# Kernel tuning notes

Hardware: AMD Instinct MI355X
Metric: run time of the kernel (lower is better)

Reference implementation:

```python
import jax, jax.numpy as jnp
from jax import lax
import numpy as np

PS = 3      # patch_size
PROP = 3    # propagate_size
DN = ('NCHW', 'OIHW', 'NCHW')


def _conv1x1(x, W, b):
    # x: [b, c, h, w]; W: [o, c]; 1x1 conv == channel matmul
    return jnp.einsum('oc,bchw->bohw', W, x) + b[None, :, None, None]


def _mpga(q_in, k_in, mask, Wq, bq, Wk, bk, Wv, bv):
    # q_in/k_in: [b, c, w, h], mask: [b, 1, w, h] (already at feature resolution)
    b, c, w, h = q_in.shape
    kp = _conv1x1(k_in, Wk, bk).reshape(b, c, w * h)          # [b, c, wh]
    qp = _conv1x1(q_in, Wq, bq).reshape(b, c, w * h)          # [b, c, wh]
    scores = jnp.einsum('bci,bcj->bij', qp, kp)               # [b, wh_q, wh_k]
    mrow = mask.reshape(b, w * h)[:, :, None]                 # mask over query rows
    A = jax.nn.softmax(scores * mrow, axis=-1)                # softmax over keys
    vp = _conv1x1(k_in, Wv, bv).reshape(b, c, w * h)
    out = jnp.einsum('bcj,bij->bci', vp, A).reshape(b, c, w, h)
    return q_in * mask + (1.0 - mask) * out


def _gap(x, m, Wq, bq, Wk, bk, Wv, bv, gamma):
    # GlobalAttentionPatch on patch stacks: x, m: [N, c, ps, ps]
    N, c, ph, pw = x.shape
    q = jnp.einsum('oc,ncij->noij', Wq, x) + bq[None, :, None, None]
    k = jnp.einsum('oc,ncij->noij', Wk, x) + bk[None, :, None, None]
    v = jnp.einsum('oc,ncij->noij', Wv, x) + bv[None, :, None, None]
    qf, kf, vf, mf = (t.reshape(N, c, ph * pw) for t in (q, k, v, m))
    cc = jnp.einsum('ncp,ndp->ncd', qf, kf)                   # [N, c, c]
    cc = jnp.einsum('ncd,ndp->ncp', cc, mf)                   # [N, c, ps*ps]
    energy = jax.nn.softmax(cc, axis=-1)
    att = (energy * vf).reshape(N, c, ph, pw)
    return x * m + gamma * (1.0 - m) * att


def _patches(x, ps):
    # torch: pad(ps//2) -> unfold(2, ps, 1).unfold(3, ps, 1) -> [b, N=w*h, c, ps, ps]
    b, c, w, h = x.shape
    p = ps // 2
    xp = jnp.pad(x, ((0, 0), (0, 0), (p, p), (p, p)))
    sl = [xp[:, :, di:di + w, dj:dj + h] for di in range(ps) for dj in range(ps)]
    pat = jnp.stack(sl, axis=-1).reshape(b, c, w, h, ps, ps)
    return pat.reshape(b, c, w * h, ps, ps).transpose(0, 2, 1, 3, 4)


def _gla_forward(foreground, mask, pf, pp, gamma):
    background = foreground * (1.0 - mask)
    fg = _mpga(foreground, background, mask, *pf)
    ck_all = _patches(background, PS)                          # [b, N, c, 3, 3]
    mk_all = _patches(jnp.broadcast_to(mask, foreground.shape), PS)
    pad = [(PS // 2, PS // 2)] * 2

    def per_sample(fm, ck, mk):
        # fm: [c, w, h]; ck, mk: [N, c, 3, 3]
        ck = ck + 1e-7
        ck = _gap(ck, mk, *pp, gamma)
        ck = ck / jnp.sqrt(jnp.sum(ck ** 2, axis=(1, 2, 3), keepdims=True))
        cr = lax.conv_general_dilated(fm[None], ck, (1, 1), pad,
                                      dimension_numbers=DN)    # [1, N, w, h]
        N = ck.shape[0]
        prop_k = jnp.ones((N, 1, PROP, PROP), fm.dtype)        # depthwise ones
        cr = lax.conv_general_dilated(cr, prop_k, (1, 1), [(1, 1), (1, 1)],
                                      dimension_numbers=DN, feature_group_count=N)
        mm = (jnp.mean(mk, axis=(1, 2, 3)) == 0.0).astype(fm.dtype)[None, :, None, None]
        att = jax.nn.softmax(cr * mm, axis=1) * mm             # softmax over N patches
        # conv_transpose2d(att, ck, stride=1, padding=1) == conv with flipped, swapped kernel
        Wt = jnp.flip(ck, (2, 3)).transpose(1, 0, 2, 3)        # [c, N, 3, 3]
        rec = lax.conv_general_dilated(att, Wt, (1, 1), pad, dimension_numbers=DN)
        return rec[0]

    return jax.vmap(per_sample)(fg, ck_all, mk_all)


def setup_inputs() -> dict:
    key = jax.random.key(0)
    ks = jax.random.split(key, 8)
    bz, nc, w, h = 2, 64, 64, 64
    s = 0.02
    foreground = jax.random.normal(ks[0], (bz, nc, w, h), jnp.float32)
    mask = jnp.zeros((bz, 1, w, h), jnp.float32).at[:, :, 16:48, 16:48].set(1.0)

    def lin(k):
        kw, kb = jax.random.split(k)
        return (jax.random.normal(kw, (nc, nc), jnp.float32) * s,
                jax.random.normal(kb, (nc,), jnp.float32) * s)

    Wq_f, bq_f = lin(ks[1]); Wk_f, bk_f = lin(ks[2]); Wv_f, bv_f = lin(ks[3])
    Wq_p, bq_p = lin(ks[4]); Wk_p, bk_p = lin(ks[5]); Wv_p, bv_p = lin(ks[6])
    return dict(foreground=foreground, mask=mask, same_number_of_args=0,
                Wq_f=Wq_f, bq_f=bq_f, Wk_f=Wk_f, bk_f=bk_f, Wv_f=Wv_f, bv_f=bv_f,
                Wq_p=Wq_p, bq_p=bq_p, Wk_p=Wk_p, bk_p=bk_p, Wv_p=Wv_p, bv_p=bv_p,
                gamma=jnp.ones((1,), jnp.float32))


def reference(foreground, mask, same_number_of_args,
              Wq_f, bq_f, Wk_f, bk_f, Wv_f, bv_f,
              Wq_p, bq_p, Wk_p, bk_p, Wv_p, bv_p, gamma):
    del same_number_of_args  # unused by the torch module as well
    pf = (Wq_f, bq_f, Wk_f, bk_f, Wv_f, bv_f)
    pp = (Wq_p, bq_p, Wk_p, bk_p, Wv_p, bv_p)
    return _gla_forward(foreground, mask, pf, pp, gamma)
```

## Files before the change

### kernel.cpp

```cpp
#include <hip/hip_runtime.h>


#define BSZ 2
#define C 64
#define WD 64
#define WH 4096
#define PW 66
#define PP 4356
#define KC 576
#define NP 4096

typedef unsigned short u16;
typedef unsigned int u32;
typedef short bf16x8 __attribute__((ext_vector_type(8)));
typedef float f32x4 __attribute__((ext_vector_type(4)));

__device__ inline u16 bf16_rne(float x) {
  unsigned u = __float_as_uint(x);
  return (u16)((u + 0x7FFFu + ((u >> 16) & 1u)) >> 16);
}
__device__ inline float bf16_tof(u16 h) { return __uint_as_float(((unsigned)h) << 16); }
__device__ inline void split2(float x, u16& h, u16& l) {
  h = bf16_rne(x);
  l = bf16_rne(x - bf16_tof(h));
}
__device__ inline u32 pack2(float x) {
  u16 h, l;
  split2(x, h, l);
  return ((u32)h << 16) | (u32)l;
}


__global__ void k_mu(const float* __restrict__ fg, const float* __restrict__ mask,
                     float* __restrict__ mu) {
  int bc = blockIdx.x;
  int b = bc >> 6;
  const float* f = fg + (size_t)bc * WH;
  const float* mk = mask + (size_t)b * WH;
  float sum = 0.f;
  for (int i = threadIdx.x; i < WH; i += 256) sum += f[i] * (1.f - mk[i]);
  __shared__ float red[256];
  red[threadIdx.x] = sum;
  __syncthreads();
  for (int s = 128; s > 0; s >>= 1) {
    if (threadIdx.x < s) red[threadIdx.x] += red[threadIdx.x + s];
    __syncthreads();
  }
  if (threadIdx.x == 0) mu[bc] = red[0] / (float)WH;
}

__global__ void k_vmean(const float* __restrict__ Wv_f, const float* __restrict__ bv_f,
                        const float* __restrict__ mu, float* __restrict__ vmean) {
  int t = threadIdx.x;
  int b = t >> 6, c = t & 63;
  float acc = bv_f[c];
  for (int cc = 0; cc < C; ++cc) acc += Wv_f[c * C + cc] * mu[b * C + cc];
  vmean[t] = acc;
}

__global__ void k_fm(const float* __restrict__ fg, const float* __restrict__ mask,
                     const float* __restrict__ vmean, float* __restrict__ fm) {
  int idx = blockIdx.x * 256 + threadIdx.x;
  if (idx >= BSZ * C * WH) return;
  int b = idx >> 18;
  int c = (idx >> 12) & 63;
  int pos = idx & (WH - 1);
  float m = mask[b * WH + pos];
  fm[idx] = fg[idx] * m + (1.f - m) * vmean[b * C + c];
}

__global__ void k_bgpT(const float* __restrict__ fg, const float* __restrict__ mask,
                       float* __restrict__ bgp) {
  int b = blockIdx.y, xp = blockIdx.x;
  float* out = bgp + ((size_t)b * PP + (size_t)xp * PW) * C;
  int t = threadIdx.x;
  __shared__ float tile[64][65];
  int xi = xp - 1;
  if (xi >= 0 && xi < WD) {
    const float* fgb = fg + (size_t)b * C * WH + (size_t)xi * WD;
    const float* mkb = mask + (size_t)b * WH + (size_t)xi * WD;
    for (int i = t; i < 64 * 64; i += 256) {
      int c = i >> 6, y = i & 63;
      tile[c][y] = fgb[(size_t)c * WH + y] * (1.f - mkb[y]);
    }
  }
  __syncthreads();
  for (int i = t; i < PW * C; i += 256) {
    int yp = i >> 6, c = i & 63;
    float v = 1e-7f;
    int yj = yp - 1;
    if (xi >= 0 && xi < WD && yj >= 0 && yj < WD) v += tile[c][yj];
    out[(size_t)yp * C + c] = v;
  }
}

__global__ void k_vgT(const float* __restrict__ bgp, const float* __restrict__ Wv_p,
                      const float* __restrict__ bv_p, float* __restrict__ Vg) {
  __shared__ float Wt[64][65];
  __shared__ float bgl[4][64];
  int t = threadIdx.x;
  for (int i = t; i < 4096; i += 256) Wt[i & 63][i >> 6] = Wv_p[i];
  int pos0 = blockIdx.x * 4;
  {
    int p2 = t >> 6, c = t & 63;
    int gp = pos0 + p2;
    bgl[p2][c] = (gp < BSZ * PP) ? bgp[(size_t)gp * C + c] : 0.f;
  }
  __syncthreads();
  int pi = t >> 6, o = t & 63;
  int gpos = pos0 + pi;
  if (gpos < BSZ * PP) {
    float acc = bv_p[o];
    for (int c = 0; c < 64; ++c) acc += Wt[c][o] * bgl[pi][c];
    Vg[(size_t)gpos * C + o] = acc;
  }
}

__global__ void k_mmf(const float* __restrict__ mask, float* __restrict__ mmf) {
  int idx = blockIdx.x * 256 + threadIdx.x;
  if (idx >= BSZ * NP) return;
  int b = idx >> 12, n = idx & 4095;
  int x = n >> 6, y = n & 63;
  float z = 0.f;
  for (int di = -1; di <= 1; ++di)
    for (int dj = -1; dj <= 1; ++dj) {
      int xi = x + di, yj = y + dj;
      if (xi >= 0 && xi < WD && yj >= 0 && yj < WD) z += mask[b * WH + xi * WD + yj];
    }
  mmf[idx] = (z == 0.f) ? 1.f : 0.f;
}

__global__ void k_scan(const float* __restrict__ mmf, int* __restrict__ lividx,
                       int* __restrict__ nliv) {
  int b = blockIdx.x, t = threadIdx.x;
  const float* mm = mmf + (size_t)b * NP;
  int* li = lividx + (size_t)b * NP;
  __shared__ int cnt[256];
  int loc[16];
  int c = 0;
#pragma unroll
  for (int i = 0; i < 16; ++i) {
    int lv = (mm[t * 16 + i] != 0.f) ? 1 : 0;
    loc[i] = lv;
    c += lv;
  }
  cnt[t] = c;
  __syncthreads();
  for (int s = 1; s < 256; s <<= 1) {
    int v = (t >= s) ? cnt[t - s] : 0;
    __syncthreads();
    cnt[t] += v;
    __syncthreads();
  }
  int base = cnt[t] - c;
#pragma unroll
  for (int i = 0; i < 16; ++i)
    if (loc[i]) li[base++] = t * 16 + i;
  int nl = cnt[255];
  if (t == 0) nliv[b] = nl;
  for (int i = nl + t; i < NP; i += 256) li[i] = 0;
}

__global__ void k_ck(const float* __restrict__ Vg, const int* __restrict__ lividx,
                     const int* __restrict__ nliv, const float* __restrict__ gamma,
                     u16* __restrict__ AkcH, u16* __restrict__ AkcL) {
  int b = blockIdx.y, nc = blockIdx.x;
  if (nc >= nliv[b]) return;
  int n = lividx[(size_t)b * NP + nc];
  int x = n >> 6, y = n & 63;
  int c = threadIdx.x;
  const float* vg = Vg + (size_t)b * PP * C;
  float g9 = gamma[0] * (1.f / 9.f);
  float o[9];
  float ss = 0.f;
#pragma unroll
  for (int p = 0; p < 9; ++p) {
    int di = p / 3, dj = p % 3;
    float v = g9 * vg[(size_t)((x + di) * PW + (y + dj)) * C + c];
    o[p] = v;
    ss += v * v;
  }
#pragma unroll
  for (int off = 32; off > 0; off >>= 1) ss += __shfl_down(ss, off, 64);
  ss = __shfl(ss, 0, 64);
  float rn = 1.f / sqrtf(ss);
  u16* ph = AkcH + ((size_t)b * NP + nc) * KC + c * 9;
  u16* pl = AkcL + ((size_t)b * NP + nc) * KC + c * 9;
#pragma unroll
  for (int p = 0; p < 9; ++p) {
    u16 h, l;
    split2(o[p] * rn, h, l);
    ph[p] = h;
    pl[p] = l;
  }
}

__global__ void k_trA(const u16* __restrict__ Sh, const u16* __restrict__ Sl,
                      u16* __restrict__ Dh, u16* __restrict__ Dl) {
  __shared__ __align__(16) u16 tile[64][72];
  int x0 = blockIdx.x * 64, k0 = blockIdx.y * 64;
  int t = threadIdx.x;
  for (int pass = 0; pass < 2; ++pass) {
    const u16* S = pass ? Sl : Sh;
    u16* D = pass ? Dl : Dh;
    for (int ch = t; ch < 512; ch += 256) {
      int r = ch >> 3, c0 = (ch & 7) * 8;
      *reinterpret_cast<uint4*>(&tile[r][c0]) =
          *reinterpret_cast<const uint4*>(S + (size_t)(x0 + r) * KC + k0 + c0);
    }
    __syncthreads();
    for (int ch = t; ch < 512; ch += 256) {
      int kr = ch >> 3, c0 = (ch & 7) * 8;
      union { u16 u[8]; uint4 v; } pk;
#pragma unroll
      for (int j = 0; j < 8; ++j) pk.u[j] = tile[c0 + j][kr];
      *reinterpret_cast<uint4*>(D + (size_t)(k0 + kr) * NP + x0 + c0) = pk.v;
    }
    __syncthreads();
  }
}

__global__ void k_im2colT(const float* __restrict__ fm, u16* __restrict__ base) {
  int ch = blockIdx.x * 256 + threadIdx.x;
  if (ch >= BSZ * WH * 72) return;
  int b = ch / (WH * 72);
  int rem = ch - b * WH * 72;
  int xy = rem / 72, kp = rem - xy * 72;
  int x = xy >> 6, y = xy & 63;
  union { u16 u[8]; uint4 v; } H, L;
#pragma unroll
  for (int j = 0; j < 8; ++j) {
    int k = kp * 8 + j;
    int c = k / 9, p = k - c * 9;
    int xi = x + p / 3 - 1, yj = y + p % 3 - 1;
    float v = 0.f;
    if (xi >= 0 && xi < WD && yj >= 0 && yj < WD)
      v = fm[((size_t)(b * C + c)) * WH + (xi << 6) + yj];
    split2(v, H.u[j], L.u[j]);
  }
  u16* bh = base + (size_t)b * 2 * WH * KC;
  u16* bl = bh + (size_t)WH * KC;
  *reinterpret_cast<uint4*>(bh + (size_t)xy * KC + kp * 8) = H.v;
  *reinterpret_cast<uint4*>(bl + (size_t)xy * KC + kp * 8) = L.v;
}


__global__ __launch_bounds__(256, 4) void k_gemmA(
    const u16* __restrict__ Ah, const u16* __restrict__ Al,
    const u16* __restrict__ Bh, const u16* __restrict__ Bl,
    const int* __restrict__ nliv, float* __restrict__ Cp) {
  int nl = *nliv;
  int m0 = blockIdx.y * 128;
  if (m0 >= nl) return;
  int n0 = blockIdx.x * 64;
  __shared__ __align__(16) u16 As[2][128][40];
  __shared__ __align__(16) u16 Bs[2][64][40];
  int t = threadIdx.x;
  f32x4 zero = {0.f, 0.f, 0.f, 0.f};
  f32x4 acc[2][4];
#pragma unroll
  for (int r = 0; r < 2; ++r)
#pragma unroll
    for (int c = 0; c < 4; ++c) acc[r][c] = zero;
  int l = t & 63, w = t >> 6;
  int lr = l & 15, lk = (l >> 4) * 8;
  for (int k0 = 0; k0 < KC; k0 += 32) {
    __syncthreads();
    for (int ch = t; ch < 1536; ch += 256) {
      const u16* src;
      u16* dst;
      if (ch < 1024) {
        int hl = ch >> 9, r = (ch >> 2) & 127, p = ch & 3;
        src = (hl ? Al : Ah) + (size_t)(m0 + r) * KC + k0 + p * 8;
        dst = &As[hl][r][p * 8];
      } else {
        int c2 = ch - 1024;
        int hl = c2 >> 8, r = (c2 >> 2) & 63, p = c2 & 3;
        src = (hl ? Bl : Bh) + (size_t)(n0 + r) * KC + k0 + p * 8;
        dst = &Bs[hl][r][p * 8];
      }
      *reinterpret_cast<uint4*>(dst) = *reinterpret_cast<const uint4*>(src);
    }
    __syncthreads();
    bf16x8 ah[2], al2[2], bh[4], bl2[4];
#pragma unroll
    for (int r = 0; r < 2; ++r) {
      ah[r] = *reinterpret_cast<const bf16x8*>(&As[0][32 * w + 16 * r + lr][lk]);
      al2[r] = *reinterpret_cast<const bf16x8*>(&As[1][32 * w + 16 * r + lr][lk]);
    }
#pragma unroll
    for (int c = 0; c < 4; ++c) {
      bh[c] = *reinterpret_cast<const bf16x8*>(&Bs[0][16 * c + lr][lk]);
      bl2[c] = *reinterpret_cast<const bf16x8*>(&Bs[1][16 * c + lr][lk]);
    }
#pragma unroll
    for (int r = 0; r < 2; ++r)
#pragma unroll
      for (int c = 0; c < 4; ++c) {
        acc[r][c] = __builtin_amdgcn_mfma_f32_16x16x32_bf16(ah[r], bh[c], acc[r][c], 0, 0, 0);
        acc[r][c] = __builtin_amdgcn_mfma_f32_16x16x32_bf16(ah[r], bl2[c], acc[r][c], 0, 0, 0);
        acc[r][c] = __builtin_amdgcn_mfma_f32_16x16x32_bf16(al2[r], bh[c], acc[r][c], 0, 0, 0);
      }
  }
#pragma unroll
  for (int r = 0; r < 2; ++r)
#pragma unroll
    for (int c = 0; c < 4; ++c)
#pragma unroll
      for (int q = 0; q < 4; ++q) {
        int row = m0 + 32 * w + 16 * r + ((l >> 4) << 2) + q;
        Cp[(size_t)row * WH + n0 + 16 * c + lr] = acc[r][c][q];
      }
}

__global__ __launch_bounds__(256, 4) void k_gemmB(
    const u16* __restrict__ Ah, const u16* __restrict__ Al,
    const u32* __restrict__ att32, const int* __restrict__ nliv,
    float* __restrict__ Cp) {
  int nl = *nliv;
  int Kend = (nl + 31) & ~31;
  int m0 = blockIdx.y * 64;
  int n0 = blockIdx.x * 64;
  __shared__ __align__(16) u16 As[2][64][40];
  __shared__ __align__(16) u16 Bs[2][64][40];
  __shared__ __align__(16) u32 Bfu[32][70];
  int t = threadIdx.x;
  f32x4 zero = {0.f, 0.f, 0.f, 0.f};
  f32x4 acc[4];
#pragma unroll
  for (int c = 0; c < 4; ++c) acc[c] = zero;
  int l = t & 63, w = t >> 6;
  int lr = l & 15, lk = (l >> 4) * 8;
  for (int k0 = 0; k0 < Kend; k0 += 32) {
    __syncthreads();
    for (int ch = t; ch < 512; ch += 256) {
      int hl = ch >> 8, r = (ch >> 2) & 63, p = ch & 3;
      const u16* src = (hl ? Al : Ah) + (size_t)(m0 + r) * NP + k0 + p * 8;
      *reinterpret_cast<uint4*>(&As[hl][r][p * 8]) = *reinterpret_cast<const uint4*>(src);
    }
    {
      int r = t >> 3, c0 = (t & 7) * 8;
      int krow = k0 + r;
      uint4 w0 = {0u, 0u, 0u, 0u}, w1 = {0u, 0u, 0u, 0u};
      if (krow < nl) {
        const u32* bp = att32 + (size_t)krow * WH + n0 + c0;
        w0 = *reinterpret_cast<const uint4*>(bp);
        w1 = *reinterpret_cast<const uint4*>(bp + 4);
      }
      Bfu[r][c0 + 0] = w0.x; Bfu[r][c0 + 1] = w0.y;
      Bfu[r][c0 + 2] = w0.z; Bfu[r][c0 + 3] = w0.w;
      Bfu[r][c0 + 4] = w1.x; Bfu[r][c0 + 5] = w1.y;
      Bfu[r][c0 + 6] = w1.z; Bfu[r][c0 + 7] = w1.w;
    }
    __syncthreads();
    {
      int n = t >> 2, kq = (t & 3) * 8;
      union { u16 u[8]; uint4 v; } H, L;
#pragma unroll
      for (int j = 0; j < 8; ++j) {
        u32 v = Bfu[kq + j][n];
        H.u[j] = (u16)(v >> 16);
        L.u[j] = (u16)(v & 0xFFFFu);
      }
      *reinterpret_cast<uint4*>(&Bs[0][n][kq]) = H.v;
      *reinterpret_cast<uint4*>(&Bs[1][n][kq]) = L.v;
    }
    __syncthreads();
    bf16x8 ah, al2, bh[4], bl2[4];
    ah = *reinterpret_cast<const bf16x8*>(&As[0][16 * w + lr][lk]);
    al2 = *reinterpret_cast<const bf16x8*>(&As[1][16 * w + lr][lk]);
#pragma unroll
    for (int c = 0; c < 4; ++c) {
      bh[c] = *reinterpret_cast<const bf16x8*>(&Bs[0][16 * c + lr][lk]);
      bl2[c] = *reinterpret_cast<const bf16x8*>(&Bs[1][16 * c + lr][lk]);
    }
#pragma unroll
    for (int c = 0; c < 4; ++c) {
      acc[c] = __builtin_amdgcn_mfma_f32_16x16x32_bf16(ah, bh[c], acc[c], 0, 0, 0);
      acc[c] = __builtin_amdgcn_mfma_f32_16x16x32_bf16(ah, bl2[c], acc[c], 0, 0, 0);
      acc[c] = __builtin_amdgcn_mfma_f32_16x16x32_bf16(al2, bh[c], acc[c], 0, 0, 0);
    }
  }
#pragma unroll
  for (int c = 0; c < 4; ++c)
#pragma unroll
    for (int q = 0; q < 4; ++q) {
      int row = m0 + 16 * w + ((l >> 4) << 2) + q;
      Cp[(size_t)row * WH + n0 + 16 * c + lr] = acc[c][q];
    }
}


__global__ __launch_bounds__(256) void k_box(const int* __restrict__ nliv,
                                             float* __restrict__ cr) {
  if ((int)blockIdx.x >= *nliv) return;
  __shared__ __align__(16) float sIn[WH];
  __shared__ __align__(16) float sT[WH];
  float* row = cr + (size_t)blockIdx.x * WH;
  const float4* r4 = reinterpret_cast<const float4*>(row);
  float4* s4 = reinterpret_cast<float4*>(sIn);
  for (int i = threadIdx.x; i < WH / 4; i += 256) s4[i] = r4[i];
  __syncthreads();
  for (int i = threadIdx.x; i < WH; i += 256) {
    int y = i & 63;
    float v = sIn[i];
    if (y > 0) v += sIn[i - 1];
    if (y < 63) v += sIn[i + 1];
    sT[i] = v;
  }
  __syncthreads();
  for (int i = threadIdx.x; i < WH; i += 256) {
    int x = i >> 6;
    float v = sT[i];
    if (x > 0) v += sT[i - 64];
    if (x < 63) v += sT[i + 64];
    row[i] = v;
  }
}

__global__ __launch_bounds__(256) void k_colstat(const float* __restrict__ cr,
                                                 const int* __restrict__ nliv,
                                                 float* __restrict__ pmax,
                                                 float* __restrict__ psum) {
  int xy = blockIdx.x * 256 + threadIdx.x;
  int nl = *nliv;
  int ns = (nl + 15) >> 4;
  int r0 = blockIdx.y * ns;
  int r1 = min(r0 + ns, nl);
  float mx = -3.4e38f, s = 0.f;
  for (int r = r0; r < r1; ++r) {
    float v = cr[(size_t)r * WH + xy];
    if (v <= mx) {
      s += __expf(v - mx);
    } else {
      s = s * __expf(mx - v) + 1.f;
      mx = v;
    }
  }
  pmax[blockIdx.y * WH + xy] = mx;
  psum[blockIdx.y * WH + xy] = s;
}

__global__ __launch_bounds__(256) void k_colmerge(const int* __restrict__ nliv,
                                                  const float* __restrict__ pmax,
                                                  const float* __restrict__ psum,
                                                  float* __restrict__ m2g,
                                                  float* __restrict__ invg) {
  int xy = blockIdx.x * 256 + threadIdx.x;
  int nl = *nliv;
  float M = -3.4e38f;
  for (int k = 0; k < 16; ++k) M = fmaxf(M, pmax[k * WH + xy]);
  float S = 0.f;
  if (M > -3.0e38f)
    for (int k = 0; k < 16; ++k) S += psum[k * WH + xy] * __expf(pmax[k * WH + xy] - M);
  int nm = NP - nl;
  float m2 = (nm > 0) ? fmaxf(M, 0.f) : M;
  float denom = (M > -3.0e38f ? S * __expf(M - m2) : 0.f) + (float)nm * __expf(-m2);
  m2g[xy] = m2;
  invg[xy] = 1.f / denom;
}

__global__ __launch_bounds__(256) void k_apply(const int* __restrict__ nliv,
                                               const float* __restrict__ m2g,
                                               const float* __restrict__ invg,
                                               float* __restrict__ cr) {
  int i = blockIdx.x * 256 + threadIdx.x;
  int row = i >> 10;
  int nl = *nliv;
  int kend = (nl + 31) & ~31;
  if (row >= kend) return;
  float4* p = reinterpret_cast<float4*>(cr) + i;
  uint4* po = reinterpret_cast<uint4*>(cr) + i;
  if (row >= nl) {
    *po = make_uint4(0u, 0u, 0u, 0u);
    return;
  }
  int xy = (i & 1023) << 2;
  float4 v = *p;
  const float4 m2 = *reinterpret_cast<const float4*>(m2g + xy);
  const float4 iv = *reinterpret_cast<const float4*>(invg + xy);
  uint4 o;
  o.x = pack2(__expf(v.x - m2.x) * iv.x);
  o.y = pack2(__expf(v.y - m2.y) * iv.y);
  o.z = pack2(__expf(v.z - m2.z) * iv.z);
  o.w = pack2(__expf(v.w - m2.w) * iv.w);
  *po = o;
}

__global__ void k_rec(const float* __restrict__ P, float* __restrict__ out) {
  int idx = blockIdx.x * 256 + threadIdx.x;
  if (idx >= BSZ * C * WH) return;
  int b = idx >> 18;
  int r = idx & 262143;
  int c = r >> 12;
  int xy = r & 4095;
  int x = xy >> 6, y = xy & 63;
  const float* Pb = P + (size_t)b * KC * WH;
  float acc = 0.f;
#pragma unroll
  for (int i = 0; i < 3; ++i) {
    int xp = x + 1 - i;
    if (xp < 0 || xp >= WD) continue;
#pragma unroll
    for (int j = 0; j < 3; ++j) {
      int yp = y + 1 - j;
      if (yp < 0 || yp >= WD) continue;
      acc += Pb[(size_t)(c * 9 + i * 3 + j) * WH + xp * WD + yp];
    }
  }
  out[idx] = acc;
}


extern "C" void kernel_launch(void* const* d_in, const int* in_sizes, int n_in,
                              void* d_out, int out_size, void* d_ws, size_t ws_size,
                              hipStream_t stream) {
  const float* fg    = (const float*)d_in[0];
  const float* mask  = (const float*)d_in[1];
  const float* Wv_f  = (const float*)d_in[7];
  const float* bv_f  = (const float*)d_in[8];
  const float* Wv_p  = (const float*)d_in[13];
  const float* bv_p  = (const float*)d_in[14];
  const float* gamma = (const float*)d_in[15];

  float* ws = (float*)d_ws;
  size_t off = 0;
  auto alloc = [&](size_t n) { size_t o = off; off += (n + 63) & ~(size_t)63; return o; };
  u16* AkcH = (u16*)(ws + alloc((size_t)BSZ * NP * KC / 2));
  u16* AkcL = (u16*)(ws + alloc((size_t)BSZ * NP * KC / 2));
  u16* AkTH = (u16*)(ws + alloc((size_t)KC * NP / 2));
  u16* AkTL = (u16*)(ws + alloc((size_t)KC * NP / 2));
  float* BimTPb = ws + alloc((size_t)BSZ * KC * WH);
  float* mmf  = ws + alloc((size_t)BSZ * NP);
  int* lividx = (int*)(ws + alloc((size_t)BSZ * NP));
  int* nliv   = (int*)(ws + alloc(64));
  float* mu   = ws + alloc(BSZ * C);
  float* vmn  = ws + alloc(BSZ * C);
  float* pmax = ws + alloc((size_t)16 * WH);
  float* psum = ws + alloc((size_t)16 * WH);
  float* m2g  = ws + alloc(WH);
  float* invg = ws + alloc(WH);
  float* cr   = ws + alloc((size_t)NP * WH);
  size_t poff = 0;
  auto palloc = [&](size_t n) { size_t o = poff; poff += (n + 63) & ~(size_t)63; return o; };
  float* bgp = cr + palloc((size_t)BSZ * PP * C);
  float* Vg  = cr + palloc((size_t)BSZ * PP * C);
  float* fmb = cr + palloc((size_t)BSZ * C * WH);
  (void)ws_size; (void)in_sizes; (void)n_in; (void)out_size;

  k_mu<<<BSZ * C, 256, 0, stream>>>(fg, mask, mu);
  k_vmean<<<1, 128, 0, stream>>>(Wv_f, bv_f, mu, vmn);
  k_fm<<<(BSZ * C * WH + 255) / 256, 256, 0, stream>>>(fg, mask, vmn, fmb);
  k_bgpT<<<dim3(PW, BSZ), 256, 0, stream>>>(fg, mask, bgp);
  k_vgT<<<(BSZ * PP + 3) / 4, 256, 0, stream>>>(bgp, Wv_p, bv_p, Vg);
  k_mmf<<<(BSZ * NP + 255) / 256, 256, 0, stream>>>(mask, mmf);
  k_scan<<<BSZ, 256, 0, stream>>>(mmf, lividx, nliv);
  k_ck<<<dim3(NP, BSZ), 64, 0, stream>>>(Vg, lividx, nliv, gamma, AkcH, AkcL);
  k_im2colT<<<(BSZ * WH * 72 + 255) / 256, 256, 0, stream>>>(fmb, (u16*)BimTPb);

  for (int b = 0; b < BSZ; ++b) {
    const u16* AkcHb = AkcH + (size_t)b * NP * KC;
    const u16* AkcLb = AkcL + (size_t)b * NP * KC;
    const u16* BimTh = (const u16*)BimTPb + (size_t)b * 2 * WH * KC;
    const u16* BimTl = BimTh + (size_t)WH * KC;
    float* Pb = BimTPb + (size_t)b * KC * WH;
    const int* nlb = nliv + b;
    k_trA<<<dim3(NP / 64, KC / 64), 256, 0, stream>>>(AkcHb, AkcLb, AkTH, AkTL);
    k_gemmA<<<dim3(WH / 64, NP / 128), 256, 0, stream>>>(AkcHb, AkcLb, BimTh, BimTl,
                                                         nlb, cr);
    k_box<<<NP, 256, 0, stream>>>(nlb, cr);
    k_colstat<<<dim3(WH / 256, 16), 256, 0, stream>>>(cr, nlb, pmax, psum);
    k_colmerge<<<WH / 256, 256, 0, stream>>>(nlb, pmax, psum, m2g, invg);
    k_apply<<<NP * (WH / 4) / 256, 256, 0, stream>>>(nlb, m2g, invg, cr);
    k_gemmB<<<dim3(WH / 64, KC / 64), 256, 0, stream>>>(AkTH, AkTL, (const u32*)cr,
                                                        nlb, Pb);
  }
  k_rec<<<(BSZ * C * WH + 255) / 256, 256, 0, stream>>>(BimTPb, (float*)d_out);
}
```

Before: 793.1 us.

## Write transposed bf16 hi/lo attention matrix and use simpler GEMM for second product

Replaces the in-place softmax apply plus the GEMM that split fp32 attention into bf16 hi/lo inside shared memory with a new kernel. That kernel computes the normalized attention, splits it into bf16 hi/lo, and writes it transposed to a separate workspace buffer. A new GEMM then loads both operands as contiguous K-major bf16 tiles. This aims to remove the per-tile conversion and strided transpose work from the GEMM inner loop. In exchange it needs an extra 64 MB workspace and a separate write/read pass, and it falls back to the old path when the workspace is too small.

```diff
diff --git a/kernel.cpp b/kernel.cpp
--- a/kernel.cpp
+++ b/kernel.cpp
@@ -311,6 +311,59 @@
         int row = m0 + 32 * w + 16 * r + ((l >> 4) << 2) + q;
         Cp[(size_t)row * WH + n0 + 16 * c + lr] = acc[r][c][q];
       }
+}
+
+__global__ __launch_bounds__(256, 4) void k_gemmB2(
+    const u16* __restrict__ Ah, const u16* __restrict__ Al,
+    const u16* __restrict__ Bh, const u16* __restrict__ Bl,
+    const int* __restrict__ nliv, float* __restrict__ Cp) {
+  int nl = *nliv;
+  int Kend = (nl + 31) & ~31;
+  int m0 = blockIdx.y * 64;
+  int n0 = blockIdx.x * 64;
+  __shared__ __align__(16) u16 As[2][64][40];
+  __shared__ __align__(16) u16 Bs[2][64][40];
+  int t = threadIdx.x;
+  f32x4 zero = {0.f, 0.f, 0.f, 0.f};
+  f32x4 acc[4];
+#pragma unroll
+  for (int c = 0; c < 4; ++c) acc[c] = zero;
+  int l = t & 63, w = t >> 6;
+  int lr = l & 15, lk = (l >> 4) * 8;
+  for (int k0 = 0; k0 < Kend; k0 += 32) {
+    __syncthreads();
+    for (int ch = t; ch < 1024; ch += 256) {
+      int sel = ch >> 9;
+      int c2 = ch & 511;
+      int hl = c2 >> 8, r = (c2 >> 2) & 63, p = c2 & 3;
+      const u16* src = sel ? ((hl ? Bl : Bh) + (size_t)(n0 + r) * NP + k0 + p * 8)
+                           : ((hl ? Al : Ah) + (size_t)(m0 + r) * NP + k0 + p * 8);
+      u16* dst = sel ? &Bs[hl][r][p * 8] : &As[hl][r][p * 8];
+      *reinterpret_cast<uint4*>(dst) = *reinterpret_cast<const uint4*>(src);
+    }
+    __syncthreads();
+    bf16x8 ah, al2, bh[4], bl2[4];
+    ah = *reinterpret_cast<const bf16x8*>(&As[0][16 * w + lr][lk]);
+    al2 = *reinterpret_cast<const bf16x8*>(&As[1][16 * w + lr][lk]);
+#pragma unroll
+    for (int c = 0; c < 4; ++c) {
+      bh[c] = *reinterpret_cast<const bf16x8*>(&Bs[0][16 * c + lr][lk]);
+      bl2[c] = *reinterpret_cast<const bf16x8*>(&Bs[1][16 * c + lr][lk]);
+    }
+#pragma unroll
+    for (int c = 0; c < 4; ++c) {
+      acc[c] = __builtin_amdgcn_mfma_f32_16x16x32_bf16(ah, bh[c], acc[c], 0, 0, 0);
+      acc[c] = __builtin_amdgcn_mfma_f32_16x16x32_bf16(ah, bl2[c], acc[c], 0, 0, 0);
+      acc[c] = __builtin_amdgcn_mfma_f32_16x16x32_bf16(al2, bh[c], acc[c], 0, 0, 0);
+    }
+  }
+#pragma unroll
+  for (int c = 0; c < 4; ++c)
+#pragma unroll
+    for (int q = 0; q < 4; ++q) {
+      int row = m0 + 16 * w + ((l >> 4) << 2) + q;
+      Cp[(size_t)row * WH + n0 + 16 * c + lr] = acc[c][q];
+    }
 }
 
 __global__ __launch_bounds__(256, 4) void k_gemmB(
@@ -458,6 +511,44 @@
   float denom = (M > -3.0e38f ? S * __expf(M - m2) : 0.f) + (float)nm * __expf(-m2);
   m2g[xy] = m2;
   invg[xy] = 1.f / denom;
+}
+
+__global__ __launch_bounds__(256) void k_applyT(const int* __restrict__ nliv,
+                                                const float* __restrict__ m2g,
+                                                const float* __restrict__ invg,
+                                                const float* __restrict__ cr,
+                                                u16* __restrict__ attT) {
+  int nl = *nliv;
+  int Kend = (nl + 31) & ~31;
+  int n0 = blockIdx.y * 64;
+  if (n0 >= Kend) return;
+  int x0 = blockIdx.x * 64;
+  __shared__ u16 Lh[64][65], Ll[64][65];
+  __shared__ float sm2[64], sinv[64];
+  int t = threadIdx.x;
+  if (t < 64) {
+    sm2[t] = m2g[x0 + t];
+    sinv[t] = invg[x0 + t];
+  }
+  __syncthreads();
+  for (int e = t; e < 4096; e += 256) {
+    int i = e >> 6, j = e & 63;
+    float v = 0.f;
+    if (n0 + i < nl)
+      v = __expf(cr[(size_t)(n0 + i) * WH + x0 + j] - sm2[j]) * sinv[j];
+    u16 h, l;
+    split2(v, h, l);
+    Lh[i][j] = h;
+    Ll[i][j] = l;
+  }
+  __syncthreads();
+  u16* p0 = attT;
+  u16* p1 = attT + (size_t)WH * NP;
+  for (int e = t; e < 4096; e += 256) {
+    int a = e >> 6, b2 = e & 63;
+    p0[(size_t)(x0 + a) * NP + n0 + b2] = Lh[b2][a];
+    p1[(size_t)(x0 + a) * NP + n0 + b2] = Ll[b2][a];
+  }
 }
 
 __global__ __launch_bounds__(256) void k_apply(const int* __restrict__ nliv,
@@ -541,12 +632,15 @@
   float* m2g  = ws + alloc(WH);
   float* invg = ws + alloc(WH);
   float* cr   = ws + alloc((size_t)NP * WH);
+  size_t attT_off = alloc((size_t)WH * NP);
+  float* attT_f = ws + attT_off;
+  bool big = (off * sizeof(float)) <= ws_size;
   size_t poff = 0;
   auto palloc = [&](size_t n) { size_t o = poff; poff += (n + 63) & ~(size_t)63; return o; };
   float* bgp = cr + palloc((size_t)BSZ * PP * C);
   float* Vg  = cr + palloc((size_t)BSZ * PP * C);
   float* fmb = cr + palloc((size_t)BSZ * C * WH);
-  (void)ws_size; (void)in_sizes; (void)n_in; (void)out_size;
+  (void)in_sizes; (void)n_in; (void)out_size;
 
   k_mu<<<BSZ * C, 256, 0, stream>>>(fg, mask, mu);
   k_vmean<<<1, 128, 0, stream>>>(Wv_f, bv_f, mu, vmn);
@@ -571,9 +665,16 @@
     k_box<<<NP, 256, 0, stream>>>(nlb, cr);
     k_colstat<<<dim3(WH / 256, 16), 256, 0, stream>>>(cr, nlb, pmax, psum);
     k_colmerge<<<WH / 256, 256, 0, stream>>>(nlb, pmax, psum, m2g, invg);
-    k_apply<<<NP * (WH / 4) / 256, 256, 0, stream>>>(nlb, m2g, invg, cr);
-    k_gemmB<<<dim3(WH / 64, KC / 64), 256, 0, stream>>>(AkTH, AkTL, (const u32*)cr,
-                                                        nlb, Pb);
+    if (big) {
+      k_applyT<<<dim3(WH / 64, NP / 64), 256, 0, stream>>>(nlb, m2g, invg, cr,
+                                                           (u16*)attT_f);
+      k_gemmB2<<<dim3(WH / 64, KC / 64), 256, 0, stream>>>(
+          AkTH, AkTL, (u16*)attT_f, (u16*)attT_f + (size_t)WH * NP, nlb, Pb);
+    } else {
+      k_apply<<<NP * (WH / 4) / 256, 256, 0, stream>>>(nlb, m2g, invg, cr);
+      k_gemmB<<<dim3(WH / 64, KC / 64), 256, 0, stream>>>(AkTH, AkTL, (const u32*)cr,
+                                                          nlb, Pb);
+    }
   }
   k_rec<<<(BSZ * C * WH + 255) / 256, 256, 0, stream>>>(BimTPb, (float*)d_out);
 }
```

Result: slower. 812.5 us (+2.4%).
